# Performance work log

Measured on AMD Instinct MI355X. Metric: run time of the kernel, lower is better.

Reference implementation:

```python
import jax, jax.numpy as jnp
import numpy as np

B, T0, H0, W0 = 8, 32, 16, 16
DV, DA, NH = 1024, 512, 16
L2 = 2048
EPS = 1e-6


def setup_inputs() -> dict:
    key = jax.random.key(0)
    ks = jax.random.split(key, 16)
    s = 0.02
    inp = {
        "video_x": jax.random.normal(ks[0], (B, T0 * H0 * W0, DV), jnp.float32),
        "audio_x": jax.random.normal(ks[1], (B, L2, DA), jnp.float32),
        "probe": jax.random.normal(ks[2], (1, 1, DV), jnp.float32) * s,
        "wq": jax.random.normal(ks[3], (DV, DV), jnp.float32) * s,
        "wk": jax.random.normal(ks[4], (DV, DV), jnp.float32) * s,
        "wv": jax.random.normal(ks[5], (DV, DV), jnp.float32) * s,
        "bq": jnp.zeros((DV,), jnp.float32),
        "bk": jnp.zeros((DV,), jnp.float32),
        "bv": jnp.zeros((DV,), jnp.float32),
        "wo": jax.random.normal(ks[6], (DV, DV), jnp.float32) * s,
        "bo": jnp.zeros((DV,), jnp.float32),
        "ln_g": jnp.ones((DV,), jnp.float32),
        "ln_b": jnp.zeros((DV,), jnp.float32),
        "proj_w": jax.random.normal(ks[7], (DA, DV), jnp.float32) * s,
        "proj_b": jnp.zeros((DA,), jnp.float32),
        "logit_scale": jnp.array([3.0], jnp.float32),
        "logit_bias": jnp.array([-3.9], jnp.float32),
        "T": T0, "H": H0, "W": W0,
    }
    return inp


def reference(video_x, audio_x, probe, wq, wk, wv, bq, bk, bv, wo, bo,
              ln_g, ln_b, proj_w, proj_b, logit_scale, logit_bias, T, H, W):
    Bv, L1, D = video_x.shape
    S = H * W
    dh = D // NH
    x = video_x.reshape(Bv, T, S, D)
    # single probe query, shared across B*T: project once
    q = (probe[0, 0] @ wq.T + bq).reshape(NH, dh)                      # [h,dh]
    k = (jnp.einsum('btsd,ed->btse', x, wk) + bk).reshape(Bv, T, S, NH, dh)
    v = (jnp.einsum('btsd,ed->btse', x, wv) + bv).reshape(Bv, T, S, NH, dh)
    scores = jnp.einsum('hd,btshd->bthcaptured'[:0] or 0, k) if False else jnp.einsum('hd,btshd->btsh', q, k) / jnp.sqrt(jnp.float32(dh))
    attn = jax.nn.softmax(scores, axis=2)                              # over S
    ctx = jnp.einsum('btsh,btshd->bthd', attn, v).reshape(Bv, T, D)
    pooled = ctx @ wo.T + bo                                           # [B,T,D]
    # LayerNorm
    mu = pooled.mean(-1, keepdims=True)
    var = ((pooled - mu) ** 2).mean(-1, keepdims=True)
    pooled = (pooled - mu) / jnp.sqrt(var + EPS) * ln_g + ln_b
    # project to audio dim, L2-normalize both sides
    vt = pooled @ proj_w.T + proj_b                                    # [B,T,Da]
    vt = vt / jnp.linalg.norm(vt, axis=-1, keepdims=True)
    a = audio_x / jnp.linalg.norm(audio_x, axis=-1, keepdims=True)
    sim = jnp.einsum('btd,bld->btl', vt, a)
    return sim * jnp.exp(logit_scale[0]) + logit_bias[0]
```

## Files before the change

kernel.cpp:

```cpp
#include <hip/hip_runtime.h>


#define FB_QWT    0u
#define FB_QB     16384u
#define FB_QF     16400u
#define FB_CTXX   18432u
#define FB_CTXP   4212736u
#define FB_POOLP  4737024u
#define FB_LNO    5261312u
#define FB_VTP    5523456u
#define FB_FLOATS 5785600u

typedef __attribute__((ext_vector_type(8))) short short8v;
typedef __attribute__((ext_vector_type(4))) float float4v;

__device__ __forceinline__ void bar_lds() {
    asm volatile("s_waitcnt lgkmcnt(0)\n\ts_barrier" ::: "memory");
}

__global__ __launch_bounds__(256) void k_qflat(const float* __restrict__ probe,
                                               const float* __restrict__ wq,
                                               const float* __restrict__ bq,
                                               float* __restrict__ qf) {
    int e = blockIdx.x, tid = threadIdx.x;
    const float* wr = wq + (size_t)e * 1024;
    float s = 0.f;
    for (int k = tid; k < 1024; k += 256) s += probe[k] * wr[k];
    s += __shfl_xor(s, 1);  s += __shfl_xor(s, 2);  s += __shfl_xor(s, 4);
    s += __shfl_xor(s, 8);  s += __shfl_xor(s, 16); s += __shfl_xor(s, 32);
    __shared__ float sm[4];
    if ((tid & 63) == 0) sm[tid >> 6] = s;
    __syncthreads();
    if (tid == 0) qf[e] = sm[0] + sm[1] + sm[2] + sm[3] + bq[e];
}

__global__ __launch_bounds__(64) void k_qwt(const float* __restrict__ qf,
                                            const float* __restrict__ wk,
                                            const float* __restrict__ bk,
                                            float* __restrict__ qwt_hd,
                                            float* __restrict__ qbs) {
    int kc = blockIdx.x, h = blockIdx.y, tid = threadIdx.x;
    int d = kc * 64 + tid;
    float s = 0.f;
    for (int e0 = 0; e0 < 64; ++e0) {
        int e = h * 64 + e0;
        s += qf[e] * wk[(size_t)e * 1024 + d];
    }
    qwt_hd[h * 1024 + d] = s * 0.125f;
    if (kc == 0) {
        float p = qf[h * 64 + tid] * bk[h * 64 + tid];
        p += __shfl_xor(p, 1);  p += __shfl_xor(p, 2);  p += __shfl_xor(p, 4);
        p += __shfl_xor(p, 8);  p += __shfl_xor(p, 16); p += __shfl_xor(p, 32);
        if (tid == 0) qbs[h] = p * 0.125f;
    }
}

__device__ __forceinline__ unsigned bf_rne(float f) {
    unsigned u = __float_as_uint(f);
    return (u + 0x7FFFu + ((u >> 16) & 1u)) >> 16;
}
__device__ __forceinline__ uint2 pack_bf4(float4 v) {
    uint2 r;
    r.x = bf_rne(v.x) | (bf_rne(v.y) << 16);
    r.y = bf_rne(v.z) | (bf_rne(v.w) << 16);
    return r;
}

__global__ __launch_bounds__(512, 2) void k1_attn(const float* __restrict__ x,
                                                  const float* __restrict__ qwt_hd,
                                                  const float* __restrict__ qbs,
                                                  float* __restrict__ ctxx) {
    __shared__ __align__(16) unsigned short xbf[16][1056];
    __shared__ __align__(16) unsigned short qwbf[16][1056];
    __shared__ __align__(16) float part[8][16][16];
    __shared__ __align__(16) float p_lds[16][16];
    __shared__ float qb_lds[16];
    __shared__ float linv_lds[16];

    const int tid  = threadIdx.x;
    const int lane = tid & 63;
    const int w    = tid >> 6;
    const int hq   = tid >> 7;
    const int cc   = tid & 127;
    const int bt   = blockIdx.x;
    const float* xb = x + (size_t)bt * 262144;

#pragma unroll
    for (int i = 0; i < 8; ++i) {
        int f4i = tid + i * 512;
        int hr = f4i >> 8, col4 = f4i & 255;
        float4 v = *(const float4*)(qwt_hd + hr * 1024 + col4 * 4);
        *(uint2*)&qwbf[hr][col4 * 4] = pack_bf4(v);
    }
    if (tid < 16) qb_lds[tid] = qbs[tid];

    float lacc = 0.f;
    float4 acc[8];
#pragma unroll
    for (int i = 0; i < 8; ++i) acc[i] = make_float4(0.f, 0.f, 0.f, 0.f);

    float4 st[8];
#pragma unroll
    for (int i = 0; i < 8; ++i)
        st[i] = *(const float4*)(xb + (size_t)(tid + i * 512) * 4);

    for (int c = 0; c < 16; ++c) {
        bar_lds();
#pragma unroll
        for (int i = 0; i < 8; ++i) {
            int f4i = tid + i * 512;
            int r = f4i >> 8, col4 = f4i & 255;
            *(uint2*)&xbf[r][col4 * 4] = pack_bf4(st[i]);
        }
        bar_lds();
        if (c < 15) {
            const float* nb = xb + (size_t)(c + 1) * 16384;
#pragma unroll
            for (int i = 0; i < 8; ++i)
                st[i] = *(const float4*)(nb + (size_t)(tid + i * 512) * 4);
        }
        {
            const int row = lane & 15;
            const int g   = lane >> 4;
            float4v cfr = {0.f, 0.f, 0.f, 0.f};
#pragma unroll
            for (int ks = 0; ks < 4; ++ks) {
                const int koff = (w * 4 + ks) * 32 + g * 8;
                short8v afr = *(const short8v*)&xbf[row][koff];
                short8v bfr = *(const short8v*)&qwbf[row][koff];
                cfr = __builtin_amdgcn_mfma_f32_16x16x32_bf16(afr, bfr, cfr, 0, 0, 0);
            }
#pragma unroll
            for (int r2 = 0; r2 < 4; ++r2)
                part[w][(lane >> 4) * 4 + r2][lane & 15] = cfr[r2];
        }
        bar_lds();
        if (tid < 256) {
            int s = tid >> 4, h = tid & 15;
            float sc = 0.f;
#pragma unroll
            for (int pw = 0; pw < 8; ++pw) sc += part[pw][s][h];
            p_lds[s][h] = __expf(sc + qb_lds[h]);
        }
        bar_lds();
        if (tid < 16) {
            float ll = 0.f;
#pragma unroll
            for (int s = 0; s < 16; ++s) ll += p_lds[s][tid];
            lacc += ll;
        }
#pragma unroll
        for (int r = 0; r < 16; ++r) {
            uint4 xv = *(const uint4*)&xbf[r][cc * 8];
            float x0 = __uint_as_float(xv.x << 16);
            float x1 = __uint_as_float(xv.x & 0xFFFF0000u);
            float x2 = __uint_as_float(xv.y << 16);
            float x3 = __uint_as_float(xv.y & 0xFFFF0000u);
            float x4 = __uint_as_float(xv.z << 16);
            float x5 = __uint_as_float(xv.z & 0xFFFF0000u);
            float x6 = __uint_as_float(xv.w << 16);
            float x7 = __uint_as_float(xv.w & 0xFFFF0000u);
            float4 p4 = *(const float4*)&p_lds[r][hq * 4];
            acc[0].x += p4.x * x0; acc[0].y += p4.x * x1; acc[0].z += p4.x * x2; acc[0].w += p4.x * x3;
            acc[1].x += p4.y * x0; acc[1].y += p4.y * x1; acc[1].z += p4.y * x2; acc[1].w += p4.y * x3;
            acc[2].x += p4.z * x0; acc[2].y += p4.z * x1; acc[2].z += p4.z * x2; acc[2].w += p4.z * x3;
            acc[3].x += p4.w * x0; acc[3].y += p4.w * x1; acc[3].z += p4.w * x2; acc[3].w += p4.w * x3;
            acc[4].x += p4.x * x4; acc[4].y += p4.x * x5; acc[4].z += p4.x * x6; acc[4].w += p4.x * x7;
            acc[5].x += p4.y * x4; acc[5].y += p4.y * x5; acc[5].z += p4.y * x6; acc[5].w += p4.y * x7;
            acc[6].x += p4.z * x4; acc[6].y += p4.z * x5; acc[6].z += p4.z * x6; acc[6].w += p4.z * x7;
            acc[7].x += p4.w * x4; acc[7].y += p4.w * x5; acc[7].z += p4.w * x6; acc[7].w += p4.w * x7;
        }
    }

    bar_lds();
    if (tid < 16) linv_lds[tid] = 1.0f / lacc;
    bar_lds();
    float* ob = ctxx + (size_t)bt * 16384;
#pragma unroll
    for (int i = 0; i < 4; ++i) {
        float li = linv_lds[hq * 4 + i];
        float4 o0 = acc[i];
        float4 o1 = acc[4 + i];
        o0.x *= li; o0.y *= li; o0.z *= li; o0.w *= li;
        o1.x *= li; o1.y *= li; o1.z *= li; o1.w *= li;
        float* dst = ob + (hq * 4 + i) * 1024 + cc * 8;
        *(float4*)dst = o0;
        *(float4*)(dst + 4) = o1;
    }
}

template<int FOLD>
__global__ __launch_bounds__(256, 2) void k_gemm2(const float* __restrict__ A0,
                                                  const float* __restrict__ A1,
                                                  const float* __restrict__ biask,
                                                  const float* __restrict__ Bw,
                                                  float* __restrict__ outp,
                                                  unsigned a_rstride, unsigned a_cstride,
                                                  unsigned ostride) {
    __shared__ __align__(16) float a_s[16][68];
    __shared__ __align__(16) float b_s[64][68];
    const int tid = threadIdx.x;
    const int rc = blockIdx.x;
    const int cb = blockIdx.y;
    const int ks = blockIdx.z;
    const int koff = ks * 512;
    const int rr = tid >> 4;
    const int ee = tid & 15;

    const size_t abase = (size_t)(rc * 16 + rr) * a_rstride + (size_t)cb * a_cstride + koff;

    float ac0 = 0.f, ac1 = 0.f, ac2 = 0.f, ac3 = 0.f;

    for (int kc = 0; kc < 8; ++kc) {
        __syncthreads();
        {
            float4 av = *(const float4*)(A0 + abase + kc * 64 + ee * 4);
            if (FOLD == 1) {
                float4 a1v = *(const float4*)(A1 + abase + kc * 64 + ee * 4);
                float4 bk4 = *(const float4*)(biask + koff + kc * 64 + ee * 4);
                av.x += a1v.x + bk4.x; av.y += a1v.y + bk4.y;
                av.z += a1v.z + bk4.z; av.w += a1v.w + bk4.w;
            }
            *(float4*)&a_s[rr][ee * 4] = av;
        }
#pragma unroll
        for (int i = 0; i < 4; ++i) {
            int f4i = tid + i * 256;
            int e = f4i >> 4, k4 = f4i & 15;
            float4 bv4 = *(const float4*)(Bw + (size_t)(cb * 64 + e) * 1024 + koff + kc * 64 + k4 * 4);
            int cs = (k4 + (e >> 2)) & 15;
            *(float4*)&b_s[e][cs * 4] = bv4;
        }
        __syncthreads();
#pragma unroll
        for (int k4 = 0; k4 < 16; ++k4) {
            float4 av = *(const float4*)&a_s[rr][k4 * 4];
            int cs = (k4 + ee) & 15;
            float4 b0 = *(const float4*)&b_s[ee * 4 + 0][cs * 4];
            float4 b1 = *(const float4*)&b_s[ee * 4 + 1][cs * 4];
            float4 b2 = *(const float4*)&b_s[ee * 4 + 2][cs * 4];
            float4 b3 = *(const float4*)&b_s[ee * 4 + 3][cs * 4];
            ac0 += av.x * b0.x + av.y * b0.y + av.z * b0.z + av.w * b0.w;
            ac1 += av.x * b1.x + av.y * b1.y + av.z * b1.z + av.w * b1.w;
            ac2 += av.x * b2.x + av.y * b2.y + av.z * b2.z + av.w * b2.w;
            ac3 += av.x * b3.x + av.y * b3.y + av.z * b3.z + av.w * b3.w;
        }
    }
    float4 o = make_float4(ac0, ac1, ac2, ac3);
    *(float4*)(outp + (size_t)ks * 256 * ostride + (size_t)(rc * 16 + rr) * ostride + cb * 64 + ee * 4) = o;
}

__global__ __launch_bounds__(256) void k_ln(const float* __restrict__ poolp,
                                            const float* __restrict__ bo,
                                            const float* __restrict__ g,
                                            const float* __restrict__ bb,
                                            float* __restrict__ out) {
    __shared__ float sm[8];
    int row = blockIdx.x, tid = threadIdx.x;
    float4 v0 = *(const float4*)(poolp + (size_t)row * 1024 + tid * 4);
    float4 v1 = *(const float4*)(poolp + 262144u + (size_t)row * 1024 + tid * 4);
    float4 bv = *(const float4*)(bo + tid * 4);
    float4 v;
    v.x = v0.x + v1.x + bv.x; v.y = v0.y + v1.y + bv.y;
    v.z = v0.z + v1.z + bv.z; v.w = v0.w + v1.w + bv.w;
    float s = v.x + v.y + v.z + v.w;
    float q = v.x * v.x + v.y * v.y + v.z * v.z + v.w * v.w;
    s += __shfl_xor(s, 1);  q += __shfl_xor(q, 1);
    s += __shfl_xor(s, 2);  q += __shfl_xor(q, 2);
    s += __shfl_xor(s, 4);  q += __shfl_xor(q, 4);
    s += __shfl_xor(s, 8);  q += __shfl_xor(q, 8);
    s += __shfl_xor(s, 16); q += __shfl_xor(q, 16);
    s += __shfl_xor(s, 32); q += __shfl_xor(q, 32);
    if ((tid & 63) == 0) { sm[tid >> 6] = s; sm[4 + (tid >> 6)] = q; }
    __syncthreads();
    float S = sm[0] + sm[1] + sm[2] + sm[3];
    float Q = sm[4] + sm[5] + sm[6] + sm[7];
    float mu = S * (1.f / 1024.f);
    float var = Q * (1.f / 1024.f) - mu * mu;
    float rs = rsqrtf(var + 1e-6f);
    float4 gg = *(const float4*)(g + tid * 4);
    float4 be = *(const float4*)(bb + tid * 4);
    float4 o;
    o.x = (v.x - mu) * rs * gg.x + be.x;
    o.y = (v.y - mu) * rs * gg.y + be.y;
    o.z = (v.z - mu) * rs * gg.z + be.z;
    o.w = (v.w - mu) * rs * gg.w + be.w;
    *(float4*)(out + (size_t)row * 1024 + tid * 4) = o;
}

__global__ __launch_bounds__(256, 2) void k_sim(const float* __restrict__ vtp,
                                                const float* __restrict__ pb,
                                                const float* __restrict__ audio,
                                                const float* __restrict__ ls,
                                                const float* __restrict__ lb,
                                                float* __restrict__ out) {
    __shared__ float a_s[64][65];
    __shared__ float v_s[32][65];
    __shared__ float rinv_a[64];
    __shared__ float rinv_v[32];
    const int tid = threadIdx.x;
    const int lc = blockIdx.x;
    const int b  = blockIdx.y;
    const int al = tid >> 2, ak = (tid & 3) * 16;
    const int vl = tid >> 3, vk = (tid & 7) * 8;
    const int rg = tid >> 4, lg = tid & 15;
    float ssa = 0.f, ssv = 0.f;
    float c00=0,c01=0,c02=0,c03=0,c10=0,c11=0,c12=0,c13=0;

    for (int kc = 0; kc < 8; ++kc) {
        __syncthreads();
        {
            const float* ap = audio + (size_t)b * 1048576 + (size_t)(lc * 64 + al) * 512 + kc * 64 + ak;
#pragma unroll
            for (int i = 0; i < 4; ++i) {
                float4 wv4 = *(const float4*)(ap + i * 4);
                ssa += wv4.x * wv4.x + wv4.y * wv4.y + wv4.z * wv4.z + wv4.w * wv4.w;
                a_s[al][ak + i * 4 + 0] = wv4.x; a_s[al][ak + i * 4 + 1] = wv4.y;
                a_s[al][ak + i * 4 + 2] = wv4.z; a_s[al][ak + i * 4 + 3] = wv4.w;
            }
            const size_t voff = (size_t)(b * 32 + vl) * 512 + kc * 64 + vk;
#pragma unroll
            for (int i = 0; i < 2; ++i) {
                float4 p0 = *(const float4*)(vtp + voff + i * 4);
                float4 p1 = *(const float4*)(vtp + 131072u + voff + i * 4);
                float4 pbv = *(const float4*)(pb + kc * 64 + vk + i * 4);
                float4 wv4;
                wv4.x = p0.x + p1.x + pbv.x; wv4.y = p0.y + p1.y + pbv.y;
                wv4.z = p0.z + p1.z + pbv.z; wv4.w = p0.w + p1.w + pbv.w;
                ssv += wv4.x * wv4.x + wv4.y * wv4.y + wv4.z * wv4.z + wv4.w * wv4.w;
                v_s[vl][vk + i * 4 + 0] = wv4.x; v_s[vl][vk + i * 4 + 1] = wv4.y;
                v_s[vl][vk + i * 4 + 2] = wv4.z; v_s[vl][vk + i * 4 + 3] = wv4.w;
            }
        }
        __syncthreads();
#pragma unroll 2
        for (int k = 0; k < 64; ++k) {
            float v0 = v_s[rg * 2 + 0][k];
            float v1 = v_s[rg * 2 + 1][k];
            float x0 = a_s[lg * 4 + 0][k];
            float x1 = a_s[lg * 4 + 1][k];
            float x2 = a_s[lg * 4 + 2][k];
            float x3 = a_s[lg * 4 + 3][k];
            c00 += v0 * x0; c01 += v0 * x1; c02 += v0 * x2; c03 += v0 * x3;
            c10 += v1 * x0; c11 += v1 * x1; c12 += v1 * x2; c13 += v1 * x3;
        }
    }
    ssa += __shfl_xor(ssa, 1); ssa += __shfl_xor(ssa, 2);
    if ((tid & 3) == 0) rinv_a[al] = rsqrtf(ssa);
    ssv += __shfl_xor(ssv, 1); ssv += __shfl_xor(ssv, 2); ssv += __shfl_xor(ssv, 4);
    if ((tid & 7) == 0) rinv_v[vl] = rsqrtf(ssv);
    __syncthreads();
    const float sc = __expf(ls[0]);
    const float bias = lb[0];
    float ra0 = rinv_a[lg * 4 + 0], ra1 = rinv_a[lg * 4 + 1];
    float ra2 = rinv_a[lg * 4 + 2], ra3 = rinv_a[lg * 4 + 3];
    float accs[2][4] = {{c00,c01,c02,c03},{c10,c11,c12,c13}};
#pragma unroll
    for (int cr = 0; cr < 2; ++cr) {
        int t = rg * 2 + cr;
        float rv = rinv_v[t] * sc;
        float4 o;
        o.x = accs[cr][0] * rv * ra0 + bias;
        o.y = accs[cr][1] * rv * ra1 + bias;
        o.z = accs[cr][2] * rv * ra2 + bias;
        o.w = accs[cr][3] * rv * ra3 + bias;
        *(float4*)(out + (size_t)b * 65536 + (size_t)t * 2048 + lc * 64 + lg * 4) = o;
    }
}

extern "C" void kernel_launch(void* const* d_in, const int* in_sizes, int n_in,
                              void* d_out, int out_size, void* d_ws, size_t ws_size,
                              hipStream_t stream) {
    (void)in_sizes; (void)n_in; (void)out_size;
    const float* video = (const float*)d_in[0];
    const float* audio = (const float*)d_in[1];
    const float* probe = (const float*)d_in[2];
    const float* wq    = (const float*)d_in[3];
    const float* wk    = (const float*)d_in[4];
    const float* wv    = (const float*)d_in[5];
    const float* bq    = (const float*)d_in[6];
    const float* bk    = (const float*)d_in[7];
    const float* bv    = (const float*)d_in[8];
    const float* wo    = (const float*)d_in[9];
    const float* bo    = (const float*)d_in[10];
    const float* lng   = (const float*)d_in[11];
    const float* lnb   = (const float*)d_in[12];
    const float* pw    = (const float*)d_in[13];
    const float* pb    = (const float*)d_in[14];
    const float* ls    = (const float*)d_in[15];
    const float* lb    = (const float*)d_in[16];
    float* ws  = (float*)d_ws;
    float* out = (float*)d_out;
    if (ws_size < FB_FLOATS * sizeof(float)) return;

    float* qwt  = ws + FB_QWT;
    float* qbs  = ws + FB_QB;
    float* qf   = ws + FB_QF;
    float* ctxx = ws + FB_CTXX;
    float* ctxp = ws + FB_CTXP;
    float* poolp= ws + FB_POOLP;
    float* lno  = ws + FB_LNO;
    float* vtp  = ws + FB_VTP;

    k_qflat<<<dim3(1024), dim3(256), 0, stream>>>(probe, wq, bq, qf);
    k_qwt<<<dim3(16, 16), dim3(64), 0, stream>>>(qf, wk, bk, qwt, qbs);
    k1_attn<<<dim3(256), dim3(512), 0, stream>>>(video, qwt, qbs, ctxx);
    k_gemm2<0><<<dim3(16, 16, 2), dim3(256), 0, stream>>>(ctxx, nullptr, nullptr, wv, ctxp,
                                                          16384u, 1024u, 1024u);
    k_gemm2<1><<<dim3(16, 16, 2), dim3(256), 0, stream>>>(ctxp, ctxp + 262144u, bv, wo, poolp,
                                                          1024u, 0u, 1024u);
    k_ln<<<dim3(256), dim3(256), 0, stream>>>(poolp, bo, lng, lnb, lno);
    k_gemm2<0><<<dim3(16, 8, 2), dim3(256), 0, stream>>>(lno, nullptr, nullptr, pw, vtp,
                                                         1024u, 0u, 512u);
    k_sim<<<dim3(32, 8), dim3(256), 0, stream>>>(vtp, pb, audio, ls, lb, out);
}
```

Measured before the change: 176.9 us.

## Software-pipeline attention chunks by deferring PV accumulation to the next iteration

Double-buffers the bf16 x tile and the softmax probability tile in LDS so that the P·V accumulation for chunk c-1 runs in the same phase as the score MFMAs for chunk c. This removes one barrier per iteration and overlaps the FMA-heavy context accumulation with the score computation. The cost is extra LDS (a second x tile of about 33KB), which may reduce occupancy below the two blocks per CU requested by the launch bounds, plus an epilogue that handles the last chunk.

```diff
diff --git a/kernel.cpp b/kernel.cpp
--- a/kernel.cpp
+++ b/kernel.cpp
@@ -70,10 +70,10 @@
                                                   const float* __restrict__ qwt_hd,
                                                   const float* __restrict__ qbs,
                                                   float* __restrict__ ctxx) {
-    __shared__ __align__(16) unsigned short xbf[16][1056];
+    __shared__ __align__(16) unsigned short xbf[2][16][1056];
     __shared__ __align__(16) unsigned short qwbf[16][1056];
     __shared__ __align__(16) float part[8][16][16];
-    __shared__ __align__(16) float p_lds[16][16];
+    __shared__ __align__(16) float p_lds[2][16][16];
     __shared__ float qb_lds[16];
     __shared__ float linv_lds[16];
 
@@ -104,13 +104,38 @@
     for (int i = 0; i < 8; ++i)
         st[i] = *(const float4*)(xb + (size_t)(tid + i * 512) * 4);
 
+#define K1_PV(PRV)                                                              \
+    _Pragma("unroll")                                                           \
+    for (int r = 0; r < 16; ++r) {                                              \
+        uint4 xv = *(const uint4*)&xbf[PRV][r][cc * 8];                         \
+        float x0 = __uint_as_float(xv.x << 16);                                 \
+        float x1 = __uint_as_float(xv.x & 0xFFFF0000u);                         \
+        float x2 = __uint_as_float(xv.y << 16);                                 \
+        float x3 = __uint_as_float(xv.y & 0xFFFF0000u);                         \
+        float x4 = __uint_as_float(xv.z << 16);                                 \
+        float x5 = __uint_as_float(xv.z & 0xFFFF0000u);                         \
+        float x6 = __uint_as_float(xv.w << 16);                                 \
+        float x7 = __uint_as_float(xv.w & 0xFFFF0000u);                         \
+        float4 p4 = *(const float4*)&p_lds[PRV][r][hq * 4];                     \
+        acc[0].x += p4.x * x0; acc[0].y += p4.x * x1; acc[0].z += p4.x * x2; acc[0].w += p4.x * x3; \
+        acc[1].x += p4.y * x0; acc[1].y += p4.y * x1; acc[1].z += p4.y * x2; acc[1].w += p4.y * x3; \
+        acc[2].x += p4.z * x0; acc[2].y += p4.z * x1; acc[2].z += p4.z * x2; acc[2].w += p4.z * x3; \
+        acc[3].x += p4.w * x0; acc[3].y += p4.w * x1; acc[3].z += p4.w * x2; acc[3].w += p4.w * x3; \
+        acc[4].x += p4.x * x4; acc[4].y += p4.x * x5; acc[4].z += p4.x * x6; acc[4].w += p4.x * x7; \
+        acc[5].x += p4.y * x4; acc[5].y += p4.y * x5; acc[5].z += p4.y * x6; acc[5].w += p4.y * x7; \
+        acc[6].x += p4.z * x4; acc[6].y += p4.z * x5; acc[6].z += p4.z * x6; acc[6].w += p4.z * x7; \
+        acc[7].x += p4.w * x4; acc[7].y += p4.w * x5; acc[7].z += p4.w * x6; acc[7].w += p4.w * x7; \
+    }
+
     for (int c = 0; c < 16; ++c) {
+        const int cur = c & 1;
+        const int prv = cur ^ 1;
         bar_lds();
 #pragma unroll
         for (int i = 0; i < 8; ++i) {
             int f4i = tid + i * 512;
             int r = f4i >> 8, col4 = f4i & 255;
-            *(uint2*)&xbf[r][col4 * 4] = pack_bf4(st[i]);
+            *(uint2*)&xbf[cur][r][col4 * 4] = pack_bf4(st[i]);
         }
         bar_lds();
         if (c < 15) {
@@ -126,13 +151,22 @@
 #pragma unroll
             for (int ks = 0; ks < 4; ++ks) {
                 const int koff = (w * 4 + ks) * 32 + g * 8;
-                short8v afr = *(const short8v*)&xbf[row][koff];
+                short8v afr = *(const short8v*)&xbf[cur][row][koff];
                 short8v bfr = *(const short8v*)&qwbf[row][koff];
                 cfr = __builtin_amdgcn_mfma_f32_16x16x32_bf16(afr, bfr, cfr, 0, 0, 0);
             }
 #pragma unroll
             for (int r2 = 0; r2 < 4; ++r2)
                 part[w][(lane >> 4) * 4 + r2][lane & 15] = cfr[r2];
+        }
+        if (c > 0) {
+            K1_PV(prv)
+            if (tid < 16) {
+                float ll = 0.f;
+#pragma unroll
+                for (int s = 0; s < 16; ++s) ll += p_lds[prv][s][tid];
+                lacc += ll;
+            }
         }
         bar_lds();
         if (tid < 256) {
@@ -140,40 +174,19 @@
             float sc = 0.f;
 #pragma unroll
             for (int pw = 0; pw < 8; ++pw) sc += part[pw][s][h];
-            p_lds[s][h] = __expf(sc + qb_lds[h]);
-        }
-        bar_lds();
-        if (tid < 16) {
-            float ll = 0.f;
-#pragma unroll
-            for (int s = 0; s < 16; ++s) ll += p_lds[s][tid];
-            lacc += ll;
-        }
-#pragma unroll
-        for (int r = 0; r < 16; ++r) {
-            uint4 xv = *(const uint4*)&xbf[r][cc * 8];
-            float x0 = __uint_as_float(xv.x << 16);
-            float x1 = __uint_as_float(xv.x & 0xFFFF0000u);
-            float x2 = __uint_as_float(xv.y << 16);
-            float x3 = __uint_as_float(xv.y & 0xFFFF0000u);
-            float x4 = __uint_as_float(xv.z << 16);
-            float x5 = __uint_as_float(xv.z & 0xFFFF0000u);
-            float x6 = __uint_as_float(xv.w << 16);
-            float x7 = __uint_as_float(xv.w & 0xFFFF0000u);
-            float4 p4 = *(const float4*)&p_lds[r][hq * 4];
-            acc[0].x += p4.x * x0; acc[0].y += p4.x * x1; acc[0].z += p4.x * x2; acc[0].w += p4.x * x3;
-            acc[1].x += p4.y * x0; acc[1].y += p4.y * x1; acc[1].z += p4.y * x2; acc[1].w += p4.y * x3;
-            acc[2].x += p4.z * x0; acc[2].y += p4.z * x1; acc[2].z += p4.z * x2; acc[2].w += p4.z * x3;
-            acc[3].x += p4.w * x0; acc[3].y += p4.w * x1; acc[3].z += p4.w * x2; acc[3].w += p4.w * x3;
-            acc[4].x += p4.x * x4; acc[4].y += p4.x * x5; acc[4].z += p4.x * x6; acc[4].w += p4.x * x7;
-            acc[5].x += p4.y * x4; acc[5].y += p4.y * x5; acc[5].z += p4.y * x6; acc[5].w += p4.y * x7;
-            acc[6].x += p4.z * x4; acc[6].y += p4.z * x5; acc[6].z += p4.z * x6; acc[6].w += p4.z * x7;
-            acc[7].x += p4.w * x4; acc[7].y += p4.w * x5; acc[7].z += p4.w * x6; acc[7].w += p4.w * x7;
+            p_lds[cur][s][h] = __expf(sc + qb_lds[h]);
         }
     }
 
     bar_lds();
-    if (tid < 16) linv_lds[tid] = 1.0f / lacc;
+    K1_PV(1)
+    if (tid < 16) {
+        float ll = 0.f;
+#pragma unroll
+        for (int s = 0; s < 16; ++s) ll += p_lds[1][s][tid];
+        lacc += ll;
+        linv_lds[tid] = 1.0f / lacc;
+    }
     bar_lds();
     float* ob = ctxx + (size_t)bt * 16384;
 #pragma unroll
@@ -187,6 +200,7 @@
         *(float4*)dst = o0;
         *(float4*)(dst + 4) = o1;
     }
+#undef K1_PV
 }
 
 template<int FOLD>
```

Measured after the change: 195.2 us. 1.1x slower.
